# Performance work log

Hardware: AMD Instinct MI355X
Metric: run time of the kernel (lower is better)

Reference implementation:

```python
import jax, jax.numpy as jnp
import numpy as np

NUM_CLASSES = 80
TOP_K = 13
ALPHA = 1.0
BETA = 6.0
EPS = 1e-9
IMG = 640


def _make_anchors(img=IMG, strides=(8, 16, 32)):
    pts = []
    for s in strides:
        n = img // s
        c = (np.arange(n, dtype=np.float32) + 0.5) * s
        yy, xx = np.meshgrid(c, c, indexing='ij')
        pts.append(np.stack([xx.ravel(), yy.ravel()], axis=-1))
    return jnp.asarray(np.concatenate(pts, 0), dtype=jnp.float32)  # [8400, 2]


def _make_boxes(key, lead_shape, img=IMG):
    k1, k2 = jax.random.split(key)
    cxcy = jax.random.uniform(k1, lead_shape + (2,), minval=0.0, maxval=float(img))
    wh = jax.random.uniform(k2, lead_shape + (2,), minval=10.0, maxval=120.0)
    return jnp.concatenate([cxcy - wh / 2, cxcy + wh / 2], axis=-1)  # xyxy


def setup_inputs() -> dict:
    key = jax.random.key(0)
    k1, k2, k3, k4 = jax.random.split(key, 4)
    bs, A, M = 32, 8400, 32
    return {
        'predict_xy_xy': _make_boxes(k1, (bs, A)),
        'predict_score': jax.random.uniform(k2, (bs, A, NUM_CLASSES)),
        'anchors_xx': _make_anchors(),
        'ground_true_labels': jax.random.randint(k3, (bs, M, 1), 0, NUM_CLASSES).astype(jnp.int64),
        'ground_true_xx_yy': _make_boxes(k4, (bs, M)),
        'mask_ground_true': jnp.ones((bs, M, 1), dtype=jnp.float32),
    }


def _pairwise_iou(gt, pd):
    # gt [b,M,4] xyxy, pd [b,A,4] xyxy -> iou [b,M,A]
    lt = jnp.maximum(gt[:, :, None, :2], pd[:, None, :, :2])
    rb = jnp.minimum(gt[:, :, None, 2:], pd[:, None, :, 2:])
    wh = jnp.clip(rb - lt, 0.0)
    inter = wh[..., 0] * wh[..., 1]
    a_gt = (gt[..., 2] - gt[..., 0]) * (gt[..., 3] - gt[..., 1])
    a_pd = (pd[..., 2] - pd[..., 0]) * (pd[..., 3] - pd[..., 1])
    union = a_gt[:, :, None] + a_pd[:, None, :] - inter
    return inter / (union + EPS)


def _assign(predict_xy_xy, predict_score, anchors_xx, gt_labels, gt_xy_xy, mask_gt):
    bs, A, C = predict_score.shape
    M = gt_xy_xy.shape[1]
    labels = gt_labels[..., 0].astype(jnp.int32)            # [b,M]
    mask_gt2 = mask_gt[..., 0]                              # [b,M] float

    # --- get_box_metrics ---
    score_t = jnp.swapaxes(predict_score, 1, 2)             # [b,C,A]
    bbox_scores = jnp.take_along_axis(score_t, labels[:, :, None], axis=1)  # [b,M,A]
    overlaps = _pairwise_iou(gt_xy_xy, predict_xy_xy)       # [b,M,A]
    align_metric = bbox_scores ** ALPHA * overlaps ** BETA  # [b,M,A]

    # --- select_candidates_in_gts: anchor center strictly inside gt box ---
    lt = anchors_xx[None, None, :, :] - gt_xy_xy[:, :, None, :2]
    rb = gt_xy_xy[:, :, None, 2:] - anchors_xx[None, None, :, :]
    deltas = jnp.concatenate([lt, rb], axis=-1)             # [b,M,A,4]
    mask_in_gts = (deltas.min(axis=-1) > EPS).astype(align_metric.dtype)  # [b,M,A]

    # --- select_top_k_candidates ---
    metrics = align_metric * mask_in_gts
    _, top_k_ids = jax.lax.top_k(metrics, TOP_K)            # [b,M,K]
    top_k_mask = mask_gt2[:, :, None] > 0                   # [b,M,1] -> broadcast
    top_k_ids = jnp.where(top_k_mask, top_k_ids, 0)
    # counts per anchor (equivalent to one_hot(...).sum(-2))
    ids_flat = top_k_ids.reshape(bs * M, TOP_K)
    counts = jnp.zeros((bs * M, A), dtype=metrics.dtype)
    counts = counts.at[jnp.arange(bs * M)[:, None], ids_flat].add(1.0)
    counts = counts.reshape(bs, M, A)
    is_in_top_k = jnp.where(counts > 1, 0.0, counts)        # drop duplicate hits

    mask_pos = is_in_top_k * mask_in_gts * mask_gt2[:, :, None]  # [b,M,A]

    # --- select_highest_overlaps (always-applied form; identity if no multi-gt) ---
    fg_mask = mask_pos.sum(axis=-2)                         # [b,A]
    mask_multi = (fg_mask[:, None, :] > 1)                  # [b,1,A] -> broadcast over M
    max_ov_idx = overlaps.argmax(axis=1)                    # [b,A]
    is_max = jax.nn.one_hot(max_ov_idx, M, dtype=overlaps.dtype)  # [b,A,M]
    is_max = jnp.swapaxes(is_max, 1, 2)                     # [b,M,A]
    mask_pos = jnp.where(mask_multi, is_max, mask_pos)
    fg_mask = mask_pos.sum(axis=-2)
    target_gt_idx = mask_pos.argmax(axis=-2)                # [b,A]

    # --- get_targets ---
    target_labels = jnp.take_along_axis(labels, target_gt_idx, axis=1)        # [b,A]
    target_xy_xy = jnp.take_along_axis(gt_xy_xy, target_gt_idx[:, :, None], axis=1)  # [b,A,4]
    target_labels = jnp.where(target_labels < 0, 0, target_labels)
    target_scores = jax.nn.one_hot(target_labels, C, dtype=predict_score.dtype)  # [b,A,C]
    target_scores = jnp.where(fg_mask[:, :, None] > 0, target_scores, 0.0)

    # --- normalization of scores by aligned metric ---
    align_metric = align_metric * mask_pos
    pos_align = align_metric.max(axis=-1, keepdims=True)    # [b,M,1]
    pos_overlaps = (overlaps * mask_pos).max(axis=-1, keepdims=True)  # [b,M,1]
    norm = (align_metric * pos_overlaps / (pos_align + EPS)).max(axis=-2)[:, :, None]  # [b,A,1]
    target_scores = target_scores * norm

    return target_labels, target_xy_xy, target_scores, fg_mask.astype(bool)


def reference(predict_xy_xy, predict_score, anchors_xx, ground_true_labels, ground_true_xx_yy, mask_ground_true):
    return _assign(predict_xy_xy, predict_score, anchors_xx,
                   ground_true_labels, ground_true_xx_yy, mask_ground_true)
```

## Files before the change

kernel.cpp:

```cpp
#include <hip/hip_runtime.h>


#define BS 32
#define A_N 8400
#define M_N 32
#define C_N 80
#define TOPK 13
#define EPSF 1e-9f
#define NSLOT (M_N * TOPK)
#define NW ((A_N + 31) / 32)
#define NBA (BS * A_N)
#define TOPK_BLKS 256
#define SCORE_BLKS 4200
#define REST_BLKS 263

typedef float vf4 __attribute__((ext_vector_type(4)));

__device__ __forceinline__ void nt_store_f4(float4 v, float4* p) {
    __builtin_nontemporal_store(*(vf4*)&v, (vf4*)p);
}

__device__ __forceinline__ float iou_f(float4 g, float4 p, float agt, float apd) {
    float lx = fmaxf(g.x, p.x), ly = fmaxf(g.y, p.y);
    float rx = fminf(g.z, p.z), ry = fminf(g.w, p.w);
    float w = fmaxf(rx - lx, 0.f), h = fmaxf(ry - ly, 0.f);
    float inter = w * h;
    return inter / (agt + apd - inter + EPSF);
}

__device__ __forceinline__ unsigned long long umax64(unsigned long long a, unsigned long long b) {
    return a > b ? a : b;
}

__global__ __launch_bounds__(256) void kZA(
    const float* __restrict__ pd, const float* __restrict__ score,
    const int* __restrict__ labels, const float* __restrict__ gt,
    const float* __restrict__ maskgt,
    int* __restrict__ cand_idx, float* __restrict__ cand_met,
    float* __restrict__ cand_ov, float* __restrict__ out)
{
    const int t = threadIdx.x;

    if (blockIdx.x >= TOPK_BLKS) {
        float* out_lbl = out;
        float* out_box = out + (size_t)NBA;
        float* out_sc  = out + (size_t)NBA * 5;
        float* out_fg  = out + (size_t)NBA * (5 + C_N);
        const unsigned fb = (unsigned)blockIdx.x - TOPK_BLKS;

        if (fb < SCORE_BLKS) {
            const unsigned base = fb * 1280u;
            float4* dst = (float4*)out_sc;
            const float4 z = make_float4(0.f, 0.f, 0.f, 0.f);
            #pragma unroll
            for (int it = 0; it < 5; ++it)
                nt_store_f4(z, &dst[base + (unsigned)it * 256u + (unsigned)t]);
        } else {
            const unsigned rb = fb - SCORE_BLKS;
            #pragma unroll
            for (int it = 0; it < 4; ++it) {
                const unsigned a = rb * 1024u + (unsigned)it * 256u + (unsigned)t;
                if (a < (unsigned)NBA) {
                    const unsigned b = a / (unsigned)A_N;
                    int l = labels[b * M_N]; if (l < 0) l = 0;
                    __builtin_nontemporal_store((float)l, &out_lbl[a]);
                    const float4 gv = ((const float4*)gt)[b * M_N];
                    nt_store_f4(gv, &((float4*)out_box)[a]);
                    __builtin_nontemporal_store(0.f, &out_fg[a]);
                }
            }
        }
        return;
    }

    const int wave = t >> 6;
    const int lane = t & 63;
    const int bm = blockIdx.x * 4 + wave;
    const int b = bm >> 5;

    if (maskgt[bm] <= 0.f) {
        if (lane < TOPK) cand_idx[bm * TOPK + lane] = -1;
        return;
    }

    const float4 g = ((const float4*)gt)[bm];
    const float agt = (g.z - g.x) * (g.w - g.y);
    const float4* pdb = (const float4*)pd + (size_t)b * A_N;
    const int lbl = labels[bm];
    const float* scb = score + (size_t)b * A_N * C_N + lbl;

    int il0, nx0, jl0, ny0, il1, nx1, jl1, ny1, il2, nx2, jl2, ny2;
    int c0, c1, c2;
    {
#define RANGE(sv, nv, lo_out, cnt_out, e_lo, e_hi)                         \
        {                                                                  \
            int lo = (int)floorf(e_lo / sv - 0.5f) - 1; lo = max(lo, 0);   \
            while (lo < nv && !(((float)lo + 0.5f) * sv > e_lo)) ++lo;     \
            int hi = (int)ceilf(e_hi / sv - 0.5f) + 1; hi = min(hi, nv-1); \
            while (hi >= 0 && !(((float)hi + 0.5f) * sv < e_hi)) --hi;     \
            lo_out = lo; cnt_out = max(hi - lo + 1, 0);                    \
        }
        RANGE(8.f, 80, il0, nx0, g.x, g.z) RANGE(8.f, 80, jl0, ny0, g.y, g.w)
        RANGE(16.f, 40, il1, nx1, g.x, g.z) RANGE(16.f, 40, jl1, ny1, g.y, g.w)
        RANGE(32.f, 20, il2, nx2, g.x, g.z) RANGE(32.f, 20, jl2, ny2, g.y, g.w)
#undef RANGE
        c0 = nx0 * ny0; c1 = nx1 * ny1; c2 = nx2 * ny2;
    }
    const int T = c0 + c1 + c2;

    unsigned long long keys[6];
    #pragma unroll
    for (int r = 0; r < 6; ++r) {
        keys[r] = 0ull;
        const int idx = r * 64 + lane;
        if (idx < T) {
            int q, n, gbase, il, jl, nx;
            if (idx < c0)           { q = idx;           n = 80; gbase = 0;    il = il0; jl = jl0; nx = nx0; }
            else if (idx < c0 + c1) { q = idx - c0;      n = 40; gbase = 6400; il = il1; jl = jl1; nx = nx1; }
            else                    { q = idx - c0 - c1; n = 20; gbase = 8000; il = il2; jl = jl2; nx = nx2; }
            const int row = q / nx, col = q - row * nx;
            const int a = gbase + (jl + row) * n + (il + col);
            float4 p = pdb[a];
            float apd = (p.z - p.x) * (p.w - p.y);
            float iou = iou_f(g, p, agt, apd);
            float sv = scb[(size_t)a * C_N];
            float i2 = iou * iou;
            float met = sv * i2 * i2 * i2;
            if (met > 0.f)
                keys[r] = ((unsigned long long)__float_as_uint(met) << 32)
                        | (unsigned)(~(unsigned)a);
        }
    }

    unsigned long long pick = 0ull;
    for (int k = 0; k < TOPK; ++k) {
        unsigned long long mx = 0ull;
        #pragma unroll
        for (int r = 0; r < 6; ++r) mx = umax64(mx, keys[r]);
        #pragma unroll
        for (int s = 32; s > 0; s >>= 1)
            mx = umax64(mx, (unsigned long long)__shfl_xor((long long)mx, s));
        if (mx == 0ull) break;
        if (lane == k) pick = mx;
        #pragma unroll
        for (int r = 0; r < 6; ++r) if (keys[r] == mx) keys[r] = 0ull;
    }

    if (lane < TOPK && pick) {
        const int a = (int)(~(unsigned)(pick & 0xFFFFFFFFu));
        const float v = __uint_as_float((unsigned)(pick >> 32));
        float4 p = pdb[a];
        float apd = (p.z - p.x) * (p.w - p.y);
        const int slot = bm * TOPK + lane;
        cand_idx[slot] = a; cand_met[slot] = v; cand_ov[slot] = iou_f(g, p, agt, apd);
    }

    const int npos = __popcll(__ballot(pick != 0ull));
    const int nfill = TOPK - npos;
    if (nfill > 0) {
        bool ing = false; float iou = 0.f, met = 0.f;
        if (lane < 32) {
            const float cx = ((float)lane + 0.5f) * 8.f, cy = 4.0f;
            ing = (cx > g.x) && (cy > g.y) && (cx < g.z) && (cy < g.w);
            if (ing) {
                float4 p = pdb[lane];
                float apd = (p.z - p.x) * (p.w - p.y);
                iou = iou_f(g, p, agt, apd);
                float i2 = iou * iou;
                met = scb[(size_t)lane * C_N] * i2 * i2 * i2;
            }
        }
        const bool z = (lane < 32) && !(met > 0.f);
        const unsigned zm32 = (unsigned)__ballot(z);
        const int ingi = ing ? 1 : 0;

        int q = lane - npos; if (q < 0) q = 0;
        unsigned mm = zm32;
        for (int i = 0; i < q; ++i) mm &= mm - 1;
        const int aq = mm ? __builtin_ctz(mm) : 0;
        const int f_ing = __shfl(ingi, aq);
        const float f_iou = __shfl(iou, aq);

        if (lane >= npos && lane < TOPK) {
            const int slot = bm * TOPK + lane;
            if (mm != 0u && f_ing) {
                cand_idx[slot] = aq; cand_met[slot] = 0.f; cand_ov[slot] = f_iou;
            } else {
                cand_idx[slot] = -1;
            }
        }
    }
}

__global__ __launch_bounds__(256) void kB_out(
    const float* __restrict__ pd, const float* __restrict__ score,
    const int* __restrict__ labels, const float* __restrict__ gt,
    const int* __restrict__ cand_idx, const float* __restrict__ cand_met,
    const float* __restrict__ cand_ov,
    float* __restrict__ out)
{
    __shared__ unsigned s_cnt[A_N];
    __shared__ int   s_sa[NSLOT];
    __shared__ float s_sm[NSLOT], s_so[NSLOT];
    __shared__ unsigned s_dd[NW];
    __shared__ float s_pal[M_N], s_pov[M_N];
    __shared__ float4 s_gt[M_N];
    __shared__ int s_lb[M_N];
    __shared__ int s_ma[NSLOT], s_mm[NSLOT];
    __shared__ float s_mal[NSLOT];
    __shared__ int s_mc;

    const int b = blockIdx.x;
    const int t = threadIdx.x;
    const size_t base = (size_t)b * A_N;

    float* out_lbl = out;
    float* out_box = out + (size_t)NBA;
    float* out_sc  = out + (size_t)NBA * 5;
    float* out_fg  = out + (size_t)NBA * (5 + C_N);

    for (int i = t; i < A_N; i += 256) s_cnt[i] = 0u;
    for (int i = t; i < NW; i += 256) s_dd[i] = 0u;
    if (t < M_N) {
        s_gt[t] = ((const float4*)gt)[b * M_N + t];
        s_lb[t] = labels[b * M_N + t];
        s_pal[t] = 0.f; s_pov[t] = 0.f;
    }
    if (t == 0) s_mc = 0;
    for (int i = t; i < NSLOT; i += 256) {
        const int gi = b * NSLOT + i;
        s_sa[i] = cand_idx[gi]; s_sm[i] = cand_met[gi]; s_so[i] = cand_ov[gi];
    }
    __syncthreads();

    for (int i = t; i < NSLOT; i += 256) {
        const int a = s_sa[i];
        if (a >= 0) atomicAdd(&s_cnt[a], 1u);
    }
    __syncthreads();

    const float4* pdb = (const float4*)pd + base;
    for (int i = t; i < NSLOT; i += 256) {
        const int a = s_sa[i];
        if (a < 0) continue;
        if (s_cnt[a] == 1u) {
            const int m = i / TOPK;
            atomicMax((int*)&s_pal[m], __float_as_int(s_sm[i]));
            atomicMax((int*)&s_pov[m], __float_as_int(s_so[i]));
        } else {
            const unsigned bit = 1u << (a & 31);
            const unsigned old = atomicOr(&s_dd[a >> 5], bit);
            if (!(old & bit)) {
                float4 p = pdb[a];
                float apd = (p.z - p.x) * (p.w - p.y);
                float best = -1.f; int bmx = 0;
                #pragma unroll
                for (int mm = 0; mm < M_N; ++mm) {
                    float4 gg = s_gt[mm];
                    float agt = (gg.z - gg.x) * (gg.w - gg.y);
                    float iou = iou_f(gg, p, agt, apd);
                    if (iou > best) { best = iou; bmx = mm; }
                }
                const float sv = score[(base + a) * C_N + s_lb[bmx]];
                const float b2 = best * best;
                const float al = sv * b2 * b2 * b2;
                const int s = atomicAdd(&s_mc, 1);
                s_ma[s] = a; s_mm[s] = bmx; s_mal[s] = al;
                atomicMax((int*)&s_pal[bmx], __float_as_int(al));
                atomicMax((int*)&s_pov[bmx], __float_as_int(best));
            }
        }
    }
    __syncthreads();

    for (int i = t; i < NSLOT; i += 256) {
        const int a = s_sa[i];
        if (a < 0 || s_cnt[a] != 1u) continue;
        const int m = i / TOPK;
        int l = s_lb[m]; if (l < 0) l = 0;
        const float nv = s_sm[i] * s_pov[m] / (s_pal[m] + EPSF);
        out_lbl[base + a] = (float)l;
        ((float4*)out_box)[base + a] = s_gt[m];
        out_fg[base + a] = 1.f;
        out_sc[(base + a) * C_N + l] = nv;
    }
    const int nm = s_mc;
    for (int i = t; i < nm; i += 256) {
        const int a = s_ma[i], m = s_mm[i];
        int l = s_lb[m]; if (l < 0) l = 0;
        const float nv = s_mal[i] * s_pov[m] / (s_pal[m] + EPSF);
        out_lbl[base + a] = (float)l;
        ((float4*)out_box)[base + a] = s_gt[m];
        out_fg[base + a] = 1.f;
        out_sc[(base + a) * C_N + l] = nv;
    }
}

extern "C" void kernel_launch(void* const* d_in, const int* in_sizes, int n_in,
                              void* d_out, int out_size, void* d_ws, size_t ws_size,
                              hipStream_t stream) {
    const float* pd      = (const float*)d_in[0];
    const float* score   = (const float*)d_in[1];
    const int*   labels  = (const int*)d_in[3];
    const float* gt      = (const float*)d_in[4];
    const float* maskgt  = (const float*)d_in[5];
    float* out = (float*)d_out;

    const int NS = BS * NSLOT;
    int*   cand_idx = (int*)d_ws;
    float* cand_met = (float*)(cand_idx + NS);
    float* cand_ov  = cand_met + NS;
    (void)ws_size; (void)in_sizes; (void)n_in;

    kZA<<<TOPK_BLKS + SCORE_BLKS + REST_BLKS, 256, 0, stream>>>(
        pd, score, labels, gt, maskgt, cand_idx, cand_met, cand_ov, out);
    kB_out<<<BS, 256, 0, stream>>>(pd, score, labels, gt,
        cand_idx, cand_met, cand_ov, out);
}
```

Baseline: 40.23 us.

## Split per-batch scatter kernel into 8 blocks with bitmask dedup

The second kernel now launches 8 blocks per batch instead of one. Each block recomputes the per-GT normalization maxima redundantly, then writes only its own eighth of the candidate slots. The per-anchor count array is replaced by two bitmasks (seen and duplicate). Deduplication picks the lowest slot index through a linear scan, which gives a deterministic owner instead of an atomic append list. This removes the large shared-memory clear of 8400 counters and exposes more parallelism for the scattered output writes. The cost is 8x redundant IoU and atomic work per batch plus an O(NSLOT) scan for each duplicate slot.

Result: slower. 58.61 us (+45.7%).

```diff
diff --git a/kernel.cpp b/kernel.cpp
--- a/kernel.cpp
+++ b/kernel.cpp
@@ -8,6 +8,7 @@
 #define TOPK 13
 #define EPSF 1e-9f
 #define NSLOT (M_N * TOPK)
+#define NPART (NSLOT / 8)
 #define NW ((A_N + 31) / 32)
 #define NBA (BS * A_N)
 #define TOPK_BLKS 256
@@ -199,18 +200,17 @@
     const float* __restrict__ cand_ov,
     float* __restrict__ out)
 {
-    __shared__ unsigned s_cnt[A_N];
     __shared__ int   s_sa[NSLOT];
     __shared__ float s_sm[NSLOT], s_so[NSLOT];
-    __shared__ unsigned s_dd[NW];
-    __shared__ float s_pal[M_N], s_pov[M_N];
+    __shared__ int   s_rm[NSLOT];
+    __shared__ float s_ral[NSLOT];
+    __shared__ unsigned s_cl[NW], s_mu[NW];
     __shared__ float4 s_gt[M_N];
     __shared__ int s_lb[M_N];
-    __shared__ int s_ma[NSLOT], s_mm[NSLOT];
-    __shared__ float s_mal[NSLOT];
-    __shared__ int s_mc;
-
-    const int b = blockIdx.x;
+    __shared__ float s_pal[M_N], s_pov[M_N];
+
+    const int b = blockIdx.x >> 3;
+    const int part = blockIdx.x & 7;
     const int t = threadIdx.x;
     const size_t base = (size_t)b * A_N;
 
@@ -219,14 +219,12 @@
     float* out_sc  = out + (size_t)NBA * 5;
     float* out_fg  = out + (size_t)NBA * (5 + C_N);
 
-    for (int i = t; i < A_N; i += 256) s_cnt[i] = 0u;
-    for (int i = t; i < NW; i += 256) s_dd[i] = 0u;
+    for (int i = t; i < NW; i += 256) { s_cl[i] = 0u; s_mu[i] = 0u; }
     if (t < M_N) {
         s_gt[t] = ((const float4*)gt)[b * M_N + t];
         s_lb[t] = labels[b * M_N + t];
         s_pal[t] = 0.f; s_pov[t] = 0.f;
     }
-    if (t == 0) s_mc = 0;
     for (int i = t; i < NSLOT; i += 256) {
         const int gi = b * NSLOT + i;
         s_sa[i] = cand_idx[gi]; s_sm[i] = cand_met[gi]; s_so[i] = cand_ov[gi];
@@ -235,64 +233,75 @@
 
     for (int i = t; i < NSLOT; i += 256) {
         const int a = s_sa[i];
-        if (a >= 0) atomicAdd(&s_cnt[a], 1u);
+        if (a >= 0) {
+            const unsigned bit = 1u << (a & 31);
+            const unsigned old = atomicOr(&s_cl[a >> 5], bit);
+            if (old & bit) atomicOr(&s_mu[a >> 5], bit);
+        }
     }
     __syncthreads();
 
     const float4* pdb = (const float4*)pd + base;
     for (int i = t; i < NSLOT; i += 256) {
         const int a = s_sa[i];
+        int rm = -1;
+        if (a >= 0) {
+            const unsigned bit = 1u << (a & 31);
+            if (!(s_mu[a >> 5] & bit)) {
+                const int m = i / TOPK;
+                atomicMax((int*)&s_pal[m], __float_as_int(s_sm[i]));
+                atomicMax((int*)&s_pov[m], __float_as_int(s_so[i]));
+                rm = -2;
+            } else {
+                int minj = i;
+                for (int j = 0; j < NSLOT; ++j)
+                    if (s_sa[j] == a && j < minj) minj = j;
+                if (minj == i) {
+                    float4 p = pdb[a];
+                    float apd = (p.z - p.x) * (p.w - p.y);
+                    float best = -1.f; int bmx = 0;
+                    #pragma unroll
+                    for (int mm = 0; mm < M_N; ++mm) {
+                        float4 gg = s_gt[mm];
+                        float agt = (gg.z - gg.x) * (gg.w - gg.y);
+                        float iou = iou_f(gg, p, agt, apd);
+                        if (iou > best) { best = iou; bmx = mm; }
+                    }
+                    const float sv = score[(base + a) * C_N + s_lb[bmx]];
+                    const float b2 = best * best;
+                    const float al = sv * b2 * b2 * b2;
+                    rm = bmx; s_ral[i] = al;
+                    atomicMax((int*)&s_pal[bmx], __float_as_int(al));
+                    atomicMax((int*)&s_pov[bmx], __float_as_int(best));
+                }
+            }
+        }
+        s_rm[i] = rm;
+    }
+    __syncthreads();
+
+    const int i0 = part * NPART;
+    for (int i = i0 + t; i < i0 + NPART; i += 256) {
+        const int a = s_sa[i];
         if (a < 0) continue;
-        if (s_cnt[a] == 1u) {
+        const int rm = s_rm[i];
+        if (rm == -2) {
             const int m = i / TOPK;
-            atomicMax((int*)&s_pal[m], __float_as_int(s_sm[i]));
-            atomicMax((int*)&s_pov[m], __float_as_int(s_so[i]));
-        } else {
-            const unsigned bit = 1u << (a & 31);
-            const unsigned old = atomicOr(&s_dd[a >> 5], bit);
-            if (!(old & bit)) {
-                float4 p = pdb[a];
-                float apd = (p.z - p.x) * (p.w - p.y);
-                float best = -1.f; int bmx = 0;
-                #pragma unroll
-                for (int mm = 0; mm < M_N; ++mm) {
-                    float4 gg = s_gt[mm];
-                    float agt = (gg.z - gg.x) * (gg.w - gg.y);
-                    float iou = iou_f(gg, p, agt, apd);
-                    if (iou > best) { best = iou; bmx = mm; }
-                }
-                const float sv = score[(base + a) * C_N + s_lb[bmx]];
-                const float b2 = best * best;
-                const float al = sv * b2 * b2 * b2;
-                const int s = atomicAdd(&s_mc, 1);
-                s_ma[s] = a; s_mm[s] = bmx; s_mal[s] = al;
-                atomicMax((int*)&s_pal[bmx], __float_as_int(al));
-                atomicMax((int*)&s_pov[bmx], __float_as_int(best));
-            }
-        }
-    }
-    __syncthreads();
-
-    for (int i = t; i < NSLOT; i += 256) {
-        const int a = s_sa[i];
-        if (a < 0 || s_cnt[a] != 1u) continue;
-        const int m = i / TOPK;
-        int l = s_lb[m]; if (l < 0) l = 0;
-        const float nv = s_sm[i] * s_pov[m] / (s_pal[m] + EPSF);
-        out_lbl[base + a] = (float)l;
-        ((float4*)out_box)[base + a] = s_gt[m];
-        out_fg[base + a] = 1.f;
-        out_sc[(base + a) * C_N + l] = nv;
-    }
-    const int nm = s_mc;
-    for (int i = t; i < nm; i += 256) {
-        const int a = s_ma[i], m = s_mm[i];
-        int l = s_lb[m]; if (l < 0) l = 0;
-        const float nv = s_mal[i] * s_pov[m] / (s_pal[m] + EPSF);
-        out_lbl[base + a] = (float)l;
-        ((float4*)out_box)[base + a] = s_gt[m];
-        out_fg[base + a] = 1.f;
-        out_sc[(base + a) * C_N + l] = nv;
+            int l = s_lb[m]; if (l < 0) l = 0;
+            const float nv = s_sm[i] * s_pov[m] / (s_pal[m] + EPSF);
+            out_lbl[base + a] = (float)l;
+            ((float4*)out_box)[base + a] = s_gt[m];
+            out_fg[base + a] = 1.f;
+            out_sc[(base + a) * C_N + l] = nv;
+        } else if (rm >= 0) {
+            const int m = rm;
+            int l = s_lb[m]; if (l < 0) l = 0;
+            const float nv = s_ral[i] * s_pov[m] / (s_pal[m] + EPSF);
+            out_lbl[base + a] = (float)l;
+            ((float4*)out_box)[base + a] = s_gt[m];
+            out_fg[base + a] = 1.f;
+            out_sc[(base + a) * C_N + l] = nv;
+        }
     }
 }
 
@@ -314,6 +323,6 @@
 
     kZA<<<TOPK_BLKS + SCORE_BLKS + REST_BLKS, 256, 0, stream>>>(
         pd, score, labels, gt, maskgt, cand_idx, cand_met, cand_ov, out);
-    kB_out<<<BS, 256, 0, stream>>>(pd, score, labels, gt,
+    kB_out<<<BS * 8, 256, 0, stream>>>(pd, score, labels, gt,
         cand_idx, cand_met, cand_ov, out);
 }
```
